# Optimization experiments

Measured on AMD Instinct MI355X. Metric: run time of the kernel, lower is better.

## Reference

```python
import jax, jax.numpy as jnp
import numpy as np

B, N, D = 8, 2048, 256
BIG = 1e9  # max_int_value used to mask the diagonal
LN_EPS = 1e-5  # F.layer_norm default eps


def setup_inputs() -> dict:
    key = jax.random.key(0)
    kq, kk = jax.random.split(key)
    q = jax.random.normal(kq, (B, N, D), dtype=jnp.float32)
    k = jax.random.normal(kk, (B, N, D), dtype=jnp.float32)
    return {"q": q, "k": k, "top_k_instances": 100, "top_k_relationships": 5}


def _forward(q, k, K, R):
    b, n, d = q.shape
    # dense QK^T + softmax over keys -> (b, n, n)
    scores1 = jax.nn.softmax(jnp.einsum('bid,bjd->bij', q, k), axis=-1)
    # instance selection: top-K of the softmaxed diagonal, sorted ascending
    diag = jnp.diagonal(scores1, axis1=-2, axis2=-1)           # (b, n)
    top_idx = jnp.sort(jax.lax.top_k(diag, K)[1], axis=-1)      # (b, K)
    # gather selected rows then selected columns -> (b, K, K)
    sel = jnp.take_along_axis(scores1, top_idx[:, :, None], axis=1)   # (b, K, n)
    rel = jnp.take_along_axis(sel, jnp.broadcast_to(top_idx[:, None, :], (b, K, K)), axis=2)
    # mask diagonal with BIG (masked_fill_ with eye)
    rel = jnp.where(jnp.eye(K, dtype=bool)[None], BIG, rel)
    # top-R relationships per selected instance; torch recovers them via
    # scatter(-1)+where, which yields row-major order with ascending column
    # indices inside each row -> equivalent to sorting top-k indices per row.
    rel_idx = jnp.sort(jax.lax.top_k(rel, R)[1], axis=-1)       # (b, K, R)
    rows = jnp.broadcast_to(jnp.arange(K)[:, None], (K, R)).reshape(-1)  # (K*R,)
    subj = top_idx[:, rows]                                     # (b, K*R) original subject ids
    obj = jnp.take_along_axis(top_idx, rel_idx.reshape(b, K * R), axis=-1)  # (b, K*R)
    batch_ids = jnp.broadcast_to(jnp.arange(b)[:, None], (b, K * R))
    soi = jnp.stack([batch_ids, subj, obj], axis=-1)            # (b, K*R, 3)
    # gather embeddings from q and layer-norm (no affine)
    se = jnp.take_along_axis(q, subj[:, :, None], axis=1)       # (b, K*R, d)
    oe = jnp.take_along_axis(q, obj[:, :, None], axis=1)
    re = se + oe
    mu = jnp.mean(re, axis=-1, keepdims=True)
    var = jnp.var(re, axis=-1, keepdims=True)
    re = (re - mu) * jax.lax.rsqrt(var + LN_EPS)
    return scores1, soi, re


def reference(q, k, top_k_instances, top_k_relationships):
    return _forward(q, k, top_k_instances, top_k_relationships)
```

## Files before the change

kernel.cpp:

```cpp
#include <hip/hip_runtime.h>
#include <math.h>

#define BB 8
#define NN 2048
#define DD 256
#define KK 100
#define RR 5
#define BIGV 1000000000.0f
#define LN_EPS 1e-5f

typedef __attribute__((ext_vector_type(8))) short short8;
typedef __attribute__((ext_vector_type(4))) float floatx4;

__device__ static inline unsigned short f2bf_rne(float x) {
  unsigned int u = __float_as_uint(x);
  unsigned int r = (u + 0x7FFFu + ((u >> 16) & 1u)) >> 16;
  return (unsigned short)r;
}
__device__ static inline float bf2f(unsigned short h) {
  return __uint_as_float(((unsigned int)h) << 16);
}

__device__ static inline void gl_lds16(const unsigned short* g, unsigned short* l) {
  __builtin_amdgcn_global_load_lds(
      (const __attribute__((address_space(1))) unsigned int*)(g),
      (__attribute__((address_space(3))) unsigned int*)(l), 16, 0, 0);
}

__global__ __launch_bounds__(256) void split_bf16(const float* __restrict__ q,
                                                  const float* __restrict__ k,
                                                  ushort4* __restrict__ qhi,
                                                  ushort4* __restrict__ qlo,
                                                  ushort4* __restrict__ khi,
                                                  ushort4* __restrict__ klo) {
  const int n4 = BB * NN * DD / 4;
  const float4* src = (blockIdx.y == 0) ? (const float4*)q : (const float4*)k;
  ushort4* hi = blockIdx.y ? khi : qhi;
  ushort4* lo = blockIdx.y ? klo : qlo;
  for (int i = blockIdx.x * 256 + threadIdx.x; i < n4; i += gridDim.x * 256) {
    float4 v = src[i];
    ushort4 h, l;
    h.x = f2bf_rne(v.x); l.x = f2bf_rne(v.x - bf2f(h.x));
    h.y = f2bf_rne(v.y); l.y = f2bf_rne(v.y - bf2f(h.y));
    h.z = f2bf_rne(v.z); l.z = f2bf_rne(v.z - bf2f(h.z));
    h.w = f2bf_rne(v.w); l.w = f2bf_rne(v.w - bf2f(h.w));
    hi[i] = h; lo[i] = l;
  }
}

__global__ __launch_bounds__(256) void gemm_mfma_split(
    const unsigned short* __restrict__ qhi, const unsigned short* __restrict__ qlo,
    const unsigned short* __restrict__ khi, const unsigned short* __restrict__ klo,
    float* __restrict__ s) {
  __shared__ unsigned short lds[2][4][8][512];

  const int lid = blockIdx.x + ((blockIdx.y + (blockIdx.z << 4)) << 4);
  const int swz = ((lid & 7) << 8) + (lid >> 3);
  const int bx = swz & 15;
  const int by = (swz >> 4) & 15;
  const int b = swz >> 8;
  const int i0 = by * 128, j0 = bx * 128;

  const int t = threadIdx.x;
  const int w = t >> 6, L = t & 63;
  const int wx = w & 1, wy = w >> 1;
  const int q_ = L >> 4, m_ = L & 15;

  const size_t bofs = (size_t)b * NN * DD;
  const unsigned short* base;
  {
    const unsigned short* b0 = qhi + bofs;
    const unsigned short* b1 = qlo + bofs;
    const unsigned short* b2 = khi + bofs;
    const unsigned short* b3 = klo + bofs;
    base = (w == 0) ? b0 : (w == 1) ? b1 : (w == 2) ? b2 : b3;
  }
  const int rowbase = (w < 2 ? i0 : j0);
  const unsigned short* gbase = base + (size_t)(rowbase + m_) * DD + q_ * 8;

  floatx4 acc[4][4];
#pragma unroll
  for (int i = 0; i < 4; ++i)
#pragma unroll
    for (int j = 0; j < 4; ++j) acc[i][j] = (floatx4){0.f, 0.f, 0.f, 0.f};

#define STAGE(buf, kb0)                                              \
  _Pragma("unroll") for (int r = 0; r < 8; ++r)                      \
      gl_lds16(gbase + (size_t)r * 16 * DD + (kb0), &lds[buf][w][r][0]);

  STAGE(0, 0);
  int cur = 0;
#pragma unroll
  for (int it = 0; it < 8; ++it) {
    if (it < 7) {
      STAGE(cur ^ 1, (it + 1) * 32);
      asm volatile("s_waitcnt vmcnt(8)" ::: "memory");
    } else {
      asm volatile("s_waitcnt vmcnt(0)" ::: "memory");
    }
    __builtin_amdgcn_s_barrier();

    short8 ah[4], al[4], bh[4], bl[4];
#pragma unroll
    for (int i = 0; i < 4; ++i) {
      ah[i] = *(const short8*)&lds[cur][0][wy * 4 + i][L * 8];
      al[i] = *(const short8*)&lds[cur][1][wy * 4 + i][L * 8];
      bh[i] = *(const short8*)&lds[cur][2][wx * 4 + i][L * 8];
      bl[i] = *(const short8*)&lds[cur][3][wx * 4 + i][L * 8];
    }
#pragma unroll
    for (int i = 0; i < 4; ++i)
#pragma unroll
      for (int j = 0; j < 4; ++j) {
        acc[i][j] = __builtin_amdgcn_mfma_f32_16x16x32_bf16(ah[i], bh[j], acc[i][j], 0, 0, 0);
        acc[i][j] = __builtin_amdgcn_mfma_f32_16x16x32_bf16(ah[i], bl[j], acc[i][j], 0, 0, 0);
        acc[i][j] = __builtin_amdgcn_mfma_f32_16x16x32_bf16(al[i], bh[j], acc[i][j], 0, 0, 0);
      }
    __builtin_amdgcn_s_barrier();
    cur ^= 1;
  }
#undef STAGE

#pragma unroll
  for (int i = 0; i < 4; ++i)
#pragma unroll
    for (int j = 0; j < 4; ++j)
#pragma unroll
      for (int r = 0; r < 4; ++r) {
        int row = i0 + wy * 64 + i * 16 + q_ * 4 + r;
        int col = j0 + wx * 64 + j * 16 + m_;
        s[((size_t)b * NN + row) * NN + col] = acc[i][j][r];
      }
}

__global__ __launch_bounds__(256) void gemm_logits(const float* __restrict__ q,
                                                   const float* __restrict__ k,
                                                   float* __restrict__ s) {
  __shared__ float As[32][132];
  __shared__ float Bs[32][132];
  const int b = blockIdx.z;
  const int i0 = blockIdx.y * 128;
  const int j0 = blockIdx.x * 128;
  const int t = threadIdx.x;
  const int tx = t & 15;
  const int ty = t >> 4;
  const float* qb = q + (size_t)b * NN * DD;
  const float* kb = k + (size_t)b * NN * DD;

  float acc[8][8];
#pragma unroll
  for (int i = 0; i < 8; ++i)
#pragma unroll
    for (int j = 0; j < 8; ++j) acc[i][j] = 0.f;

  for (int kb0 = 0; kb0 < DD; kb0 += 32) {
#pragma unroll
    for (int l = 0; l < 4; ++l) {
      int f = l * 256 + t;
      int row = f >> 3;
      int c4 = (f & 7) * 4;
      float4 va = *(const float4*)(qb + (size_t)(i0 + row) * DD + kb0 + c4);
      float4 vb = *(const float4*)(kb + (size_t)(j0 + row) * DD + kb0 + c4);
      As[c4 + 0][row] = va.x; As[c4 + 1][row] = va.y;
      As[c4 + 2][row] = va.z; As[c4 + 3][row] = va.w;
      Bs[c4 + 0][row] = vb.x; Bs[c4 + 1][row] = vb.y;
      Bs[c4 + 2][row] = vb.z; Bs[c4 + 3][row] = vb.w;
    }
    __syncthreads();
#pragma unroll
    for (int kk = 0; kk < 32; ++kk) {
      float a[8], bv[8];
      *(float4*)&a[0] = *(const float4*)&As[kk][ty * 8];
      *(float4*)&a[4] = *(const float4*)&As[kk][ty * 8 + 4];
      *(float4*)&bv[0] = *(const float4*)&Bs[kk][tx * 8];
      *(float4*)&bv[4] = *(const float4*)&Bs[kk][tx * 8 + 4];
#pragma unroll
      for (int i = 0; i < 8; ++i)
#pragma unroll
        for (int j = 0; j < 8; ++j) acc[i][j] += a[i] * bv[j];
    }
    __syncthreads();
  }

#pragma unroll
  for (int i = 0; i < 8; ++i) {
    size_t row = (size_t)(i0 + ty * 8 + i);
    float* po = s + ((size_t)b * NN + row) * NN + j0 + tx * 8;
    *(float4*)po = make_float4(acc[i][0], acc[i][1], acc[i][2], acc[i][3]);
    *(float4*)(po + 4) = make_float4(acc[i][4], acc[i][5], acc[i][6], acc[i][7]);
  }
}

__device__ inline float pick4(float4 v, int j) {
  return j == 0 ? v.x : (j == 1 ? v.y : (j == 2 ? v.z : v.w));
}

__global__ __launch_bounds__(256) void softmax_rows(float* __restrict__ s,
                                                    float* __restrict__ diag) {
  const int bi = blockIdx.x;
  const int irow = bi & (NN - 1);
  const int t = threadIdx.x;
  float4* rowp = (float4*)(s + (size_t)bi * NN);
  float4 v0 = rowp[t];
  float4 v1 = rowp[256 + t];

  __shared__ float red[4];
  float m = fmaxf(fmaxf(fmaxf(v0.x, v0.y), fmaxf(v0.z, v0.w)),
                  fmaxf(fmaxf(v1.x, v1.y), fmaxf(v1.z, v1.w)));
#pragma unroll
  for (int off = 32; off; off >>= 1) m = fmaxf(m, __shfl_xor(m, off));
  if ((t & 63) == 0) red[t >> 6] = m;
  __syncthreads();
  m = fmaxf(fmaxf(red[0], red[1]), fmaxf(red[2], red[3]));
  __syncthreads();

  float4 e0, e1;
  e0.x = expf(v0.x - m); e0.y = expf(v0.y - m);
  e0.z = expf(v0.z - m); e0.w = expf(v0.w - m);
  e1.x = expf(v1.x - m); e1.y = expf(v1.y - m);
  e1.z = expf(v1.z - m); e1.w = expf(v1.w - m);
  float sum = e0.x + e0.y + e0.z + e0.w + e1.x + e1.y + e1.z + e1.w;
#pragma unroll
  for (int off = 32; off; off >>= 1) sum += __shfl_xor(sum, off);
  if ((t & 63) == 0) red[t >> 6] = sum;
  __syncthreads();
  sum = red[0] + red[1] + red[2] + red[3];

  float inv = 1.0f / sum;
  float4 s0 = make_float4(e0.x * inv, e0.y * inv, e0.z * inv, e0.w * inv);
  float4 s1 = make_float4(e1.x * inv, e1.y * inv, e1.z * inv, e1.w * inv);
  rowp[t] = s0;
  rowp[256 + t] = s1;

  int c0 = t * 4;
  if (irow >= c0 && irow < c0 + 4) diag[bi] = pick4(s0, irow - c0);
  int c1 = 1024 + t * 4;
  if (irow >= c1 && irow < c1 + 4) diag[bi] = pick4(s1, irow - c1);
}

__global__ __launch_bounds__(1024) void topk_diag(const float* __restrict__ diag,
                                                  int* __restrict__ topidx) {
  const int b = blockIdx.x;
  const int t = threadIdx.x;
  __shared__ unsigned long long key[NN];
  __shared__ int idxs[KK];

#pragma unroll
  for (int sIt = 0; sIt < 2; ++sIt) {
    int i = t + sIt * 1024;
    unsigned int vb = __float_as_uint(diag[b * NN + i]);
    key[i] = ((unsigned long long)vb << 32) | (unsigned int)(NN - 1 - i);
  }
  __syncthreads();

  for (int kstep = 2; kstep <= NN; kstep <<= 1) {
    for (int j = kstep >> 1; j > 0; j >>= 1) {
      int i = ((t & ~(j - 1)) << 1) | (t & (j - 1));
      int l = i | j;
      unsigned long long a = key[i];
      unsigned long long c = key[l];
      bool desc = ((i & kstep) == 0);
      if (desc ? (a < c) : (a > c)) { key[i] = c; key[l] = a; }
      __syncthreads();
    }
  }

  if (t < KK) idxs[t] = NN - 1 - (int)(unsigned int)(key[t] & 0xFFFFFFFFu);
  __syncthreads();
  if (t < KK) {
    int myidx = idxs[t];
    int rank = 0;
#pragma unroll 4
    for (int j = 0; j < KK; ++j) rank += (idxs[j] < myidx) ? 1 : 0;
    topidx[b * KK + rank] = myidx;
  }
}

__global__ __launch_bounds__(64) void rel_topk(const float* __restrict__ s,
                                               const int* __restrict__ topidx,
                                               float* __restrict__ soi,
                                               int2* __restrict__ pairs) {
  const int b = blockIdx.y;
  const int i = blockIdx.x;
  const int l = threadIdx.x;
  const int* tixb = topidx + b * KK;
  const int subj = tixb[i];
  const float* srow = s + ((size_t)b * NN + subj) * NN;

  const int j0 = l, j1 = l + 64;
  int c0 = tixb[j0];
  float v0 = (j0 == i) ? BIGV : srow[c0];
  unsigned long long k0 =
      ((unsigned long long)__float_as_uint(v0) << 32) | (unsigned int)(KK - 1 - j0);
  unsigned long long k1 = 0ull;
  if (j1 < KK) {
    int c1 = tixb[j1];
    float v1 = (j1 == i) ? BIGV : srow[c1];
    k1 = ((unsigned long long)__float_as_uint(v1) << 32) | (unsigned int)(KK - 1 - j1);
  }

  int sel[RR];
#pragma unroll
  for (int r = 0; r < RR; ++r) {
    unsigned long long best = k0 > k1 ? k0 : k1;
#pragma unroll
    for (int off = 32; off; off >>= 1) {
      unsigned long long o = __shfl_xor(best, off);
      if (o > best) best = o;
    }
    int js = KK - 1 - (int)(unsigned int)(best & 0xFFFFFFFFull);
    sel[r] = js;
    if (j0 == js) k0 = 0ull;
    if (j1 == js) k1 = 0ull;
  }

  if (l == 0) {
#pragma unroll
    for (int a2 = 0; a2 < RR; ++a2)
#pragma unroll
      for (int b2 = a2 + 1; b2 < RR; ++b2)
        if (sel[b2] < sel[a2]) { int tmp = sel[a2]; sel[a2] = sel[b2]; sel[b2] = tmp; }
#pragma unroll
    for (int r = 0; r < RR; ++r) {
      int obj = tixb[sel[r]];
      size_t p = ((size_t)b * KK + i) * RR + r;
      soi[p * 3 + 0] = (float)b;
      soi[p * 3 + 1] = (float)subj;
      soi[p * 3 + 2] = (float)obj;
      pairs[p] = make_int2(subj, obj);
    }
  }
}

__global__ __launch_bounds__(64) void edge_ln(const float* __restrict__ q,
                                              const int2* __restrict__ pairs,
                                              float* __restrict__ re) {
  const int p = blockIdx.x;
  const int b = p / (KK * RR);
  const int l = threadIdx.x;
  int2 pr = pairs[p];
  const float4* qs = (const float4*)(q + ((size_t)b * NN + pr.x) * DD);
  const float4* qo = (const float4*)(q + ((size_t)b * NN + pr.y) * DD);
  float4 a = qs[l];
  float4 o = qo[l];
  a.x += o.x; a.y += o.y; a.z += o.z; a.w += o.w;
  float sum = a.x + a.y + a.z + a.w;
  float sq = a.x * a.x + a.y * a.y + a.z * a.z + a.w * a.w;
#pragma unroll
  for (int off = 32; off; off >>= 1) {
    sum += __shfl_xor(sum, off);
    sq += __shfl_xor(sq, off);
  }
  float mu = sum * (1.f / DD);
  float var = sq * (1.f / DD) - mu * mu;
  float rs = rsqrtf(var + LN_EPS);
  float4 r4 = make_float4((a.x - mu) * rs, (a.y - mu) * rs,
                          (a.z - mu) * rs, (a.w - mu) * rs);
  ((float4*)(re + (size_t)p * DD))[l] = r4;
}

extern "C" void kernel_launch(void* const* d_in, const int* in_sizes, int n_in,
                              void* d_out, int out_size, void* d_ws, size_t ws_size,
                              hipStream_t stream) {
  const float* q = (const float*)d_in[0];
  const float* k = (const float*)d_in[1];

  float* out = (float*)d_out;
  float* scores = out;
  float* soi = out + (size_t)BB * NN * NN;
  float* re = soi + (size_t)BB * KK * RR * 3;

  char* ws = (char*)d_ws;
  float* diag = (float*)ws;
  int* topidx = (int*)(ws + (size_t)BB * NN * 4);
  int2* pairs = (int2*)(ws + (size_t)BB * NN * 4 + (size_t)BB * KK * 4);
  const size_t small_end = 128 * 1024;
  const size_t plane = (size_t)BB * NN * DD * 2;
  const bool use_mfma = ws_size >= small_end + 4 * plane;

  if (use_mfma) {
    unsigned short* qhi = (unsigned short*)(ws + small_end);
    unsigned short* qlo = (unsigned short*)(ws + small_end + plane);
    unsigned short* khi = (unsigned short*)(ws + small_end + 2 * plane);
    unsigned short* klo = (unsigned short*)(ws + small_end + 3 * plane);
    split_bf16<<<dim3(1024, 2), 256, 0, stream>>>(q, k, (ushort4*)qhi, (ushort4*)qlo,
                                                  (ushort4*)khi, (ushort4*)klo);
    gemm_mfma_split<<<dim3(NN / 128, NN / 128, BB), 256, 0, stream>>>(qhi, qlo, khi, klo,
                                                                      scores);
  } else {
    gemm_logits<<<dim3(NN / 128, NN / 128, BB), 256, 0, stream>>>(q, k, scores);
  }
  softmax_rows<<<dim3(BB * NN), 256, 0, stream>>>(scores, diag);
  topk_diag<<<dim3(BB), 1024, 0, stream>>>(diag, topidx);
  rel_topk<<<dim3(KK, BB), 64, 0, stream>>>(scores, topidx, soi, pairs);
  edge_ln<<<dim3(BB * KK * RR), 64, 0, stream>>>(q, pairs, re);
}
```

Before: 281.7 us.

## Replace per-batch bitonic sort top-K with parallel rank counting and ballot compaction

```diff
diff --git a/kernel.cpp b/kernel.cpp
--- a/kernel.cpp
+++ b/kernel.cpp
@@ -238,41 +238,58 @@
   if (irow >= c1 && irow < c1 + 4) diag[bi] = pick4(s1, irow - c1);
 }
 
-__global__ __launch_bounds__(1024) void topk_diag(const float* __restrict__ diag,
-                                                  int* __restrict__ topidx) {
+__global__ __launch_bounds__(256) void topk_rank(const float* __restrict__ diag,
+                                                 unsigned char* __restrict__ flags) {
+  const int b = blockIdx.y;
+  const int c = blockIdx.x;
+  const int t = threadIdx.x;
+  __shared__ unsigned long long key[NN];
+  __shared__ unsigned short partial[256];
+
+#pragma unroll
+  for (int sIt = 0; sIt < 8; ++sIt) {
+    int i = t + sIt * 256;
+    unsigned int vb = __float_as_uint(diag[b * NN + i]);
+    key[i] = ((unsigned long long)vb << 32) | (unsigned int)(NN - 1 - i);
+  }
+  __syncthreads();
+
+  const int e = c * 128 + (t & 127);
+  const int base = (t >> 7) * 1024;
+  const unsigned long long my = key[e];
+  int r = 0;
+#pragma unroll 8
+  for (int j = 0; j < 1024; ++j) r += (key[base + j] > my) ? 1 : 0;
+  partial[t] = (unsigned short)r;
+  __syncthreads();
+
+  if (t < 128) {
+    int rank = (int)partial[t] + (int)partial[t + 128];
+    flags[b * NN + e] = (rank < KK) ? 1 : 0;
+  }
+}
+
+__global__ __launch_bounds__(1024) void topk_compact(const unsigned char* __restrict__ flags,
+                                                     int* __restrict__ topidx) {
   const int b = blockIdx.x;
   const int t = threadIdx.x;
-  __shared__ unsigned long long key[NN];
-  __shared__ int idxs[KK];
-
-#pragma unroll
-  for (int sIt = 0; sIt < 2; ++sIt) {
-    int i = t + sIt * 1024;
-    unsigned int vb = __float_as_uint(diag[b * NN + i]);
-    key[i] = ((unsigned long long)vb << 32) | (unsigned int)(NN - 1 - i);
-  }
-  __syncthreads();
-
-  for (int kstep = 2; kstep <= NN; kstep <<= 1) {
-    for (int j = kstep >> 1; j > 0; j >>= 1) {
-      int i = ((t & ~(j - 1)) << 1) | (t & (j - 1));
-      int l = i | j;
-      unsigned long long a = key[i];
-      unsigned long long c = key[l];
-      bool desc = ((i & kstep) == 0);
-      if (desc ? (a < c) : (a > c)) { key[i] = c; key[l] = a; }
-      __syncthreads();
-    }
-  }
-
-  if (t < KK) idxs[t] = NN - 1 - (int)(unsigned int)(key[t] & 0xFFFFFFFFu);
-  __syncthreads();
-  if (t < KK) {
-    int myidx = idxs[t];
-    int rank = 0;
-#pragma unroll 4
-    for (int j = 0; j < KK; ++j) rank += (idxs[j] < myidx) ? 1 : 0;
-    topidx[b * KK + rank] = myidx;
+  __shared__ unsigned long long mask[32];
+  const bool f0 = flags[b * NN + t] != 0;
+  const bool f1 = flags[b * NN + t + 1024] != 0;
+  const unsigned long long m0 = __ballot(f0);
+  const unsigned long long m1 = __ballot(f1);
+  const int w = t >> 6, l = t & 63;
+  if (l == 0) { mask[w] = m0; mask[16 + w] = m1; }
+  __syncthreads();
+  if (f0) {
+    int pos = __popcll(m0 & ((1ull << l) - 1ull));
+    for (int j = 0; j < w; ++j) pos += __popcll(mask[j]);
+    topidx[b * KK + pos] = t;
+  }
+  if (f1) {
+    int pos = __popcll(m1 & ((1ull << l) - 1ull));
+    for (int j = 0; j < 16 + w; ++j) pos += __popcll(mask[j]);
+    topidx[b * KK + pos] = t + 1024;
   }
 }
 
@@ -374,6 +391,9 @@
   float* diag = (float*)ws;
   int* topidx = (int*)(ws + (size_t)BB * NN * 4);
   int2* pairs = (int2*)(ws + (size_t)BB * NN * 4 + (size_t)BB * KK * 4);
+  unsigned char* flags =
+      (unsigned char*)(ws + (size_t)BB * NN * 4 + (size_t)BB * KK * 4 +
+                       (size_t)BB * KK * RR * 8);
   const size_t small_end = 128 * 1024;
   const size_t plane = (size_t)BB * NN * DD * 2;
   const bool use_mfma = ws_size >= small_end + 4 * plane;
@@ -391,7 +411,8 @@
     gemm_logits<<<dim3(NN / 128, NN / 128, BB), 256, 0, stream>>>(q, k, scores);
   }
   softmax_rows<<<dim3(BB * NN), 256, 0, stream>>>(scores, diag);
-  topk_diag<<<dim3(BB), 1024, 0, stream>>>(diag, topidx);
+  topk_rank<<<dim3(16, BB), 256, 0, stream>>>(diag, flags);
+  topk_compact<<<dim3(BB), 1024, 0, stream>>>(flags, topidx);
   rel_topk<<<dim3(KK, BB), 64, 0, stream>>>(scores, topidx, soi, pairs);
   edge_ln<<<dim3(BB * KK * RR), 64, 0, stream>>>(q, pairs, re);
 }
```

New measurement: 281.1 us. Within noise of the previous version (-0.2%).
